# Kernel optimization log

Measured on AMD Instinct MI355X. Metric: run time of the kernel, lower is better.

Reference implementation:

```python
import jax, jax.numpy as jnp
import numpy as np

IN_FEATURES = 4096
OUT_FEATURES = 4096
N_TOKENS = 8192


def setup_inputs() -> dict:
    key = jax.random.key(0)
    kx, kw = jax.random.split(key)
    x = jax.random.normal(kx, (N_TOKENS, IN_FEATURES), dtype=jnp.float32)
    # weight = randn(out, in) * 0.1, bias = zeros(out), per BinaryLinear.__init__
    weight = jax.random.normal(kw, (OUT_FEATURES, IN_FEATURES), dtype=jnp.float32) * 0.1
    bias = jnp.zeros((OUT_FEATURES,), dtype=jnp.float32)
    return {"x": x, "weight": weight, "bias": bias}


def reference(x, weight, bias):
    # sign-binarize weights (torch .sign(): -1/0/+1, matched by jnp.sign),
    # then dense linear: x @ sign(W)^T + b
    bin_w = jnp.sign(weight)
    return jnp.einsum('ni,oi->no', x, bin_w) + bias
```

## Files before the change

kernel.cpp:

```cpp
#include <hip/hip_runtime.h>
#include <stdint.h>

typedef __attribute__((ext_vector_type(4)))  int i32x4;
typedef __attribute__((ext_vector_type(16))) int i32x16;

#define M_TOK 8192
#define N_OUT 4096
#define K_IN  4096

#define BM 128
#define BN 128
#define BK 128

#define GLDS16(gp, lp)                                                         \
  __builtin_amdgcn_global_load_lds(                                            \
      (const __attribute__((address_space(1))) void*)(gp),                     \
      (__attribute__((address_space(3))) void*)(lp), 16, 0, 0)

__global__ void __launch_bounds__(256) quant_x_i8(const float* __restrict__ x,
                                                  char* __restrict__ xq,
                                                  float* __restrict__ scales) {
  const int row = blockIdx.x;
  const int t   = threadIdx.x;
  const float4* rp = (const float4*)(x + (size_t)row * K_IN);

  float4 v[4];
#pragma unroll
  for (int p = 0; p < 4; p++) v[p] = rp[p * 256 + t];

  float amax = 0.f;
#pragma unroll
  for (int p = 0; p < 4; p++)
    amax = fmaxf(amax, fmaxf(fmaxf(fabsf(v[p].x), fabsf(v[p].y)),
                             fmaxf(fabsf(v[p].z), fabsf(v[p].w))));

#pragma unroll
  for (int off = 32; off > 0; off >>= 1)
    amax = fmaxf(amax, __shfl_xor(amax, off));

  __shared__ float wmax[4];
  if ((t & 63) == 0) wmax[t >> 6] = amax;
  __syncthreads();
  amax = fmaxf(fmaxf(wmax[0], wmax[1]), fmaxf(wmax[2], wmax[3]));
  amax = fmaxf(amax, 1e-30f);

  const float inv = 127.f / amax;
  if (t == 0) scales[row] = amax / 127.f;

  uint32_t* op = (uint32_t*)(xq + (size_t)row * K_IN);
#pragma unroll
  for (int p = 0; p < 4; p++) {
    uint32_t b0 = (uint32_t)(__float2int_rn(v[p].x * inv) & 0xFF);
    uint32_t b1 = (uint32_t)(__float2int_rn(v[p].y * inv) & 0xFF);
    uint32_t b2 = (uint32_t)(__float2int_rn(v[p].z * inv) & 0xFF);
    uint32_t b3 = (uint32_t)(__float2int_rn(v[p].w * inv) & 0xFF);
    op[p * 256 + t] = b0 | (b1 << 8) | (b2 << 16) | (b3 << 24);
  }
}

__global__ void __launch_bounds__(256) quant_w_sign(const float* __restrict__ w,
                                                    char* __restrict__ wq) {
  const int t = threadIdx.x;
  const size_t base = (size_t)blockIdx.x * 1024;
  const float4* p = (const float4*)w + base;
  uint32_t* op = (uint32_t*)wq + base;
#pragma unroll
  for (int q = 0; q < 4; q++) {
    float4 f = p[q * 256 + t];
    int s0 = (f.x > 0.f) - (f.x < 0.f);
    int s1 = (f.y > 0.f) - (f.y < 0.f);
    int s2 = (f.z > 0.f) - (f.z < 0.f);
    int s3 = (f.w > 0.f) - (f.w < 0.f);
    op[q * 256 + t] = (uint32_t)(s0 & 0xFF) | ((uint32_t)(s1 & 0xFF) << 8) |
                      ((uint32_t)(s2 & 0xFF) << 16) | ((uint32_t)(s3 & 0xFF) << 24);
  }
}

__global__ void __launch_bounds__(256) gemm_bin_i8(
    const char* __restrict__ A, const char* __restrict__ B,
    const float* __restrict__ scales, const float* __restrict__ bias,
    float* __restrict__ C) {
  __shared__ char sA[BM * BK];
  __shared__ char sB[BN * BK];

  const int tid  = threadIdx.x;
  const int lane = tid & 63;
  const int wv   = tid >> 6;
  const int wr   = wv >> 1;
  const int wc   = wv & 1;

  const int m0 = blockIdx.y * BM;
  const int n0 = blockIdx.x * BN;

  const int srow   = lane >> 3;
  const int schunk = (lane & 7) ^ srow;
  const char* gA = A + (size_t)(m0 + wv * 32 + srow) * K_IN + schunk * 16;
  const char* gB = B + (size_t)(n0 + wv * 32 + srow) * K_IN + schunk * 16;
  char* lA = &sA[(wv * 32) * BK];
  char* lB = &sB[(wv * 32) * BK];

  i32x16 acc[2][2];
#pragma unroll
  for (int i = 0; i < 2; i++)
#pragma unroll
    for (int j = 0; j < 2; j++)
#pragma unroll
      for (int r = 0; r < 16; r++) acc[i][j][r] = 0;

  const int fr  = lane & 31;
  const int k16 = lane >> 5;
  const int x7  = lane & 7;
  const char* rA = &sA[(wr * 64 + fr) * BK];
  const char* rB = &sB[(wc * 64 + fr) * BK];

  for (int k0 = 0; k0 < K_IN; k0 += BK) {
#pragma unroll
    for (int g = 0; g < 4; g++) {
      GLDS16(gA + k0 + (size_t)(g * 8) * K_IN, lA + g * 8 * BK);
      GLDS16(gB + k0 + (size_t)(g * 8) * K_IN, lB + g * 8 * BK);
    }
    __syncthreads();

#pragma unroll
    for (int ks = 0; ks < 4; ks++) {
      const int soff = ((ks * 2 + k16) ^ x7) << 4;
      i32x4 aF[2], bF[2];
      aF[0] = *(const i32x4*)(rA + soff);
      aF[1] = *(const i32x4*)(rA + 32 * BK + soff);
      bF[0] = *(const i32x4*)(rB + soff);
      bF[1] = *(const i32x4*)(rB + 32 * BK + soff);
#pragma unroll
      for (int mi = 0; mi < 2; mi++)
#pragma unroll
        for (int ni = 0; ni < 2; ni++)
          acc[mi][ni] = __builtin_amdgcn_mfma_i32_32x32x32_i8(
              aF[mi], bF[ni], acc[mi][ni], 0, 0, 0);
    }
    __syncthreads();
  }

#pragma unroll
  for (int ni = 0; ni < 2; ni++) {
    const int col = n0 + wc * 64 + ni * 32 + (lane & 31);
    const float bv = bias[col];
#pragma unroll
    for (int mi = 0; mi < 2; mi++) {
      const int rbase = m0 + wr * 64 + mi * 32 + (lane >> 5) * 4;
#pragma unroll
      for (int r = 0; r < 16; r++) {
        const int row = rbase + (r & 3) + 8 * (r >> 2);
        C[(size_t)row * N_OUT + col] = (float)acc[mi][ni][r] * scales[row] + bv;
      }
    }
  }
}

__global__ void fallback_gemm(const float* __restrict__ x, const float* __restrict__ w,
                              const float* __restrict__ bias, float* __restrict__ out) {
  int idx = blockIdx.x * blockDim.x + threadIdx.x;
  if (idx >= M_TOK * N_OUT) return;
  int row = idx / N_OUT, col = idx % N_OUT;
  const float* xp = x + (size_t)row * K_IN;
  const float* wp = w + (size_t)col * K_IN;
  float s = 0.f;
  for (int k = 0; k < K_IN; k++) {
    float wv = wp[k];
    float sg = wv > 0.f ? 1.f : (wv < 0.f ? -1.f : 0.f);
    s += xp[k] * sg;
  }
  out[idx] = s + bias[col];
}

extern "C" void kernel_launch(void* const* d_in, const int* in_sizes, int n_in,
                              void* d_out, int out_size, void* d_ws, size_t ws_size,
                              hipStream_t stream) {
  const float* x    = (const float*)d_in[0];
  const float* w    = (const float*)d_in[1];
  const float* bias = (const float*)d_in[2];
  float* out = (float*)d_out;

  const size_t xq_bytes = (size_t)M_TOK * K_IN;
  const size_t wq_bytes = (size_t)N_OUT * K_IN;
  const size_t sc_bytes = (size_t)M_TOK * sizeof(float);

  if (ws_size < xq_bytes + wq_bytes + sc_bytes) {
    int total = M_TOK * N_OUT;
    fallback_gemm<<<(total + 255) / 256, 256, 0, stream>>>(x, w, bias, out);
    return;
  }

  char*  xq = (char*)d_ws;
  char*  wq = (char*)d_ws + xq_bytes;
  float* sc = (float*)((char*)d_ws + xq_bytes + wq_bytes);

  quant_x_i8<<<M_TOK, 256, 0, stream>>>(x, xq, sc);
  quant_w_sign<<<(N_OUT * K_IN / 4) / 1024, 256, 0, stream>>>(w, wq);

  dim3 grid(N_OUT / BN, M_TOK / BM);
  gemm_bin_i8<<<grid, 256, 0, stream>>>(xq, wq, sc, bias, out);
}
```

Baseline: 404.5 us.

## Restructure int8 GEMM into 256x256 tiles with 4-stage LDS pipeline

Grows the GEMM block tile to 256x256 with 512 threads, each wave computing a 128x64 subtile, and shrinks the K step to 64. Adds a four-slot LDS ring buffer filled with global_load_lds three tiles ahead, using vmcnt waits and a single barrier per step so loads overlap MFMA work. Also remaps block IDs into a grouped order for L2 reuse and raises MFMA issue priority with setprio. The 128 KB of LDS and the larger accumulator set limit occupancy, and launch_bounds(512,2) may not be met.

```diff
diff --git a/kernel.cpp b/kernel.cpp
--- a/kernel.cpp
+++ b/kernel.cpp
@@ -8,9 +8,12 @@
 #define N_OUT 4096
 #define K_IN  4096
 
-#define BM 128
-#define BN 128
-#define BK 128
+#define BM 256
+#define BN 256
+#define BKB 64
+#define NT (K_IN / BKB)
+#define SLOT_BYTES 32768
+#define B_OFF 16384
 
 #define GLDS16(gp, lp)                                                         \
   __builtin_amdgcn_global_load_lds(                                            \
@@ -76,81 +79,114 @@
   }
 }
 
-__global__ void __launch_bounds__(256) gemm_bin_i8(
+__global__ void __launch_bounds__(512, 2) gemm_bin_i8(
     const char* __restrict__ A, const char* __restrict__ B,
     const float* __restrict__ scales, const float* __restrict__ bias,
     float* __restrict__ C) {
-  __shared__ char sA[BM * BK];
-  __shared__ char sB[BN * BK];
+  __shared__ __align__(16) char lds[4 * SLOT_BYTES];
 
   const int tid  = threadIdx.x;
   const int lane = tid & 63;
   const int wv   = tid >> 6;
-  const int wr   = wv >> 1;
-  const int wc   = wv & 1;
-
-  const int m0 = blockIdx.y * BM;
-  const int n0 = blockIdx.x * BN;
-
-  const int srow   = lane >> 3;
-  const int schunk = (lane & 7) ^ srow;
-  const char* gA = A + (size_t)(m0 + wv * 32 + srow) * K_IN + schunk * 16;
-  const char* gB = B + (size_t)(n0 + wv * 32 + srow) * K_IN + schunk * 16;
-  char* lA = &sA[(wv * 32) * BK];
-  char* lB = &sB[(wv * 32) * BK];
-
-  i32x16 acc[2][2];
-#pragma unroll
-  for (int i = 0; i < 2; i++)
-#pragma unroll
-    for (int j = 0; j < 2; j++)
-#pragma unroll
-      for (int r = 0; r < 16; r++) acc[i][j][r] = 0;
+  const int wm   = wv >> 2;
+  const int wn   = wv & 3;
+
+  int bid = (int)blockIdx.x;
+  bid = (bid & 7) * (512 >> 3) + (bid >> 3);
+  const int m0 = (bid >> 4) * BM;
+  const int n0 = (bid & 15) * BN;
+
+  const int srow   = lane >> 2;
+  const int schunk = (lane & 3) ^ ((lane >> 3) & 3);
+  const char* gAb = A + (size_t)(m0 + wv * 32 + srow) * K_IN + schunk * 16;
+  const char* gBb = B + (size_t)(n0 + wv * 32 + srow) * K_IN + schunk * 16;
+  char* lAb = lds + wv * 2048;
+  char* lBb = lds + B_OFF + wv * 2048;
+
+  auto stage = [&](int tt, int sl) {
+    const size_t ko = (size_t)tt * BKB;
+    GLDS16(gAb + ko,                     lAb + sl * SLOT_BYTES);
+    GLDS16(gAb + ko + (size_t)16 * K_IN, lAb + sl * SLOT_BYTES + 1024);
+    GLDS16(gBb + ko,                     lBb + sl * SLOT_BYTES);
+    GLDS16(gBb + ko + (size_t)16 * K_IN, lBb + sl * SLOT_BYTES + 1024);
+  };
 
   const int fr  = lane & 31;
   const int k16 = lane >> 5;
-  const int x7  = lane & 7;
-  const char* rA = &sA[(wr * 64 + fr) * BK];
-  const char* rB = &sB[(wc * 64 + fr) * BK];
-
-  for (int k0 = 0; k0 < K_IN; k0 += BK) {
-#pragma unroll
-    for (int g = 0; g < 4; g++) {
-      GLDS16(gA + k0 + (size_t)(g * 8) * K_IN, lA + g * 8 * BK);
-      GLDS16(gB + k0 + (size_t)(g * 8) * K_IN, lB + g * 8 * BK);
+  const int x3  = (lane >> 1) & 3;
+  const int aoff = wm * 8192 + fr * 64;
+  const int boff = B_OFF + wn * 4096 + fr * 64;
+
+  i32x16 acc[4][2];
+#pragma unroll
+  for (int m = 0; m < 4; m++)
+#pragma unroll
+    for (int n = 0; n < 2; n++)
+#pragma unroll
+      for (int r = 0; r < 16; r++) acc[m][n][r] = 0;
+
+  auto compute = [&](int sl) {
+    const char* pA = lds + sl * SLOT_BYTES + aoff;
+    const char* pB = lds + sl * SLOT_BYTES + boff;
+#pragma unroll
+    for (int ks = 0; ks < 2; ks++) {
+      const int so = ((2 * ks + k16) ^ x3) << 4;
+      i32x4 a0 = *(const i32x4*)(pA + so);
+      i32x4 a1 = *(const i32x4*)(pA + 2048 + so);
+      i32x4 a2 = *(const i32x4*)(pA + 4096 + so);
+      i32x4 a3 = *(const i32x4*)(pA + 6144 + so);
+      i32x4 b0 = *(const i32x4*)(pB + so);
+      i32x4 b1 = *(const i32x4*)(pB + 2048 + so);
+      __builtin_amdgcn_s_setprio(1);
+      acc[0][0] = __builtin_amdgcn_mfma_i32_32x32x32_i8(a0, b0, acc[0][0], 0, 0, 0);
+      acc[0][1] = __builtin_amdgcn_mfma_i32_32x32x32_i8(a0, b1, acc[0][1], 0, 0, 0);
+      acc[1][0] = __builtin_amdgcn_mfma_i32_32x32x32_i8(a1, b0, acc[1][0], 0, 0, 0);
+      acc[1][1] = __builtin_amdgcn_mfma_i32_32x32x32_i8(a1, b1, acc[1][1], 0, 0, 0);
+      acc[2][0] = __builtin_amdgcn_mfma_i32_32x32x32_i8(a2, b0, acc[2][0], 0, 0, 0);
+      acc[2][1] = __builtin_amdgcn_mfma_i32_32x32x32_i8(a2, b1, acc[2][1], 0, 0, 0);
+      acc[3][0] = __builtin_amdgcn_mfma_i32_32x32x32_i8(a3, b0, acc[3][0], 0, 0, 0);
+      acc[3][1] = __builtin_amdgcn_mfma_i32_32x32x32_i8(a3, b1, acc[3][1], 0, 0, 0);
+      __builtin_amdgcn_s_setprio(0);
     }
-    __syncthreads();
-
-#pragma unroll
-    for (int ks = 0; ks < 4; ks++) {
-      const int soff = ((ks * 2 + k16) ^ x7) << 4;
-      i32x4 aF[2], bF[2];
-      aF[0] = *(const i32x4*)(rA + soff);
-      aF[1] = *(const i32x4*)(rA + 32 * BK + soff);
-      bF[0] = *(const i32x4*)(rB + soff);
-      bF[1] = *(const i32x4*)(rB + 32 * BK + soff);
-#pragma unroll
-      for (int mi = 0; mi < 2; mi++)
-#pragma unroll
-        for (int ni = 0; ni < 2; ni++)
-          acc[mi][ni] = __builtin_amdgcn_mfma_i32_32x32x32_i8(
-              aF[mi], bF[ni], acc[mi][ni], 0, 0, 0);
-    }
-    __syncthreads();
-  }
-
-#pragma unroll
-  for (int ni = 0; ni < 2; ni++) {
-    const int col = n0 + wc * 64 + ni * 32 + (lane & 31);
-    const float bv = bias[col];
-#pragma unroll
-    for (int mi = 0; mi < 2; mi++) {
-      const int rbase = m0 + wr * 64 + mi * 32 + (lane >> 5) * 4;
-#pragma unroll
-      for (int r = 0; r < 16; r++) {
-        const int row = rbase + (r & 3) + 8 * (r >> 2);
-        C[(size_t)row * N_OUT + col] = (float)acc[mi][ni][r] * scales[row] + bv;
-      }
+  };
+
+  stage(0, 0);
+  stage(1, 1);
+  stage(2, 2);
+
+  for (int t = 0; t < NT - 3; ++t) {
+    asm volatile("s_waitcnt vmcnt(8)" ::: "memory");
+    __builtin_amdgcn_s_barrier();
+    __builtin_amdgcn_sched_barrier(0);
+    stage(t + 3, (t + 3) & 3);
+    compute(t & 3);
+  }
+  asm volatile("s_waitcnt vmcnt(8)" ::: "memory");
+  __builtin_amdgcn_s_barrier();
+  __builtin_amdgcn_sched_barrier(0);
+  compute((NT - 3) & 3);
+  asm volatile("s_waitcnt vmcnt(4)" ::: "memory");
+  __builtin_amdgcn_s_barrier();
+  __builtin_amdgcn_sched_barrier(0);
+  compute((NT - 2) & 3);
+  asm volatile("s_waitcnt vmcnt(0)" ::: "memory");
+  __builtin_amdgcn_s_barrier();
+  __builtin_amdgcn_sched_barrier(0);
+  compute((NT - 1) & 3);
+
+  const int col0 = n0 + wn * 64 + (lane & 31);
+  const float bv0 = bias[col0];
+  const float bv1 = bias[col0 + 32];
+#pragma unroll
+  for (int m = 0; m < 4; m++) {
+    const int rb = m0 + wm * 128 + m * 32 + ((lane >> 5) << 2);
+#pragma unroll
+    for (int r = 0; r < 16; r++) {
+      const int row = rb + (r & 3) + ((r >> 2) << 3);
+      const float sc = scales[row];
+      float* cp = C + (size_t)row * N_OUT + col0;
+      cp[0]  = (float)acc[m][0][r] * sc + bv0;
+      cp[32] = (float)acc[m][1][r] * sc + bv1;
     }
   }
 }
@@ -196,6 +232,5 @@
   quant_x_i8<<<M_TOK, 256, 0, stream>>>(x, xq, sc);
   quant_w_sign<<<(N_OUT * K_IN / 4) / 1024, 256, 0, stream>>>(w, wq);
 
-  dim3 grid(N_OUT / BN, M_TOK / BM);
-  gemm_bin_i8<<<grid, 256, 0, stream>>>(xq, wq, sc, bias, out);
-}
+  gemm_bin_i8<<<512, 512, 0, stream>>>(xq, wq, sc, bias, out);
+}
```

New measurement: 396.1 us. 2.1% less time.
